# Performance work log

Hardware: AMD Instinct MI355X
Metric: run time of the kernel (lower is better)

## Reference

```python
import jax, jax.numpy as jnp
import numpy as np

N_NODES = 100000
N_EDGES = 1600000
DIM = 128


def setup_inputs() -> dict:
    key = jax.random.key(0)
    ks = jax.random.split(key, 8)
    s = 1.0 / np.sqrt(DIM)
    return {
        "x": jax.random.normal(ks[0], (N_NODES, DIM), dtype=jnp.float32),
        "edge_index": jax.random.randint(ks[1], (2, N_EDGES), 0, N_NODES, dtype=jnp.int64),
        "W1_l": jax.random.normal(ks[2], (DIM, DIM), dtype=jnp.float32) * s,
        "b1": jnp.zeros((DIM,), dtype=jnp.float32),
        "W1_r": jax.random.normal(ks[3], (DIM, DIM), dtype=jnp.float32) * s,
        "W2_l": jax.random.normal(ks[4], (DIM, DIM), dtype=jnp.float32) * s,
        "b2": jnp.zeros((DIM,), dtype=jnp.float32),
        "W2_r": jax.random.normal(ks[5], (DIM, DIM), dtype=jnp.float32) * s,
    }


def _sage_conv(h, src, dst, n, W_l, b, W_r):
    # mean aggregation of source-node features onto target nodes
    agg = jax.ops.segment_sum(h[src], dst, num_segments=n)          # [N, D]
    deg = jax.ops.segment_sum(jnp.ones_like(src, dtype=h.dtype), dst, num_segments=n)
    agg = agg / jnp.maximum(deg, 1.0)[:, None]
    # PyG SAGEConv: lin_l(aggr) + bias + lin_r(x)  (root weight, no bias on lin_r)
    return agg @ W_l + b + h @ W_r


def reference(x, edge_index, W1_l, b1, W1_r, W2_l, b2, W2_r):
    src, dst = edge_index[0], edge_index[1]
    n = x.shape[0]
    h = jax.nn.relu(_sage_conv(x, src, dst, n, W1_l, b1, W1_r))
    return _sage_conv(h, src, dst, n, W2_l, b2, W2_r)
```

## Files before the change

### kernel.cpp

```cpp
#include <hip/hip_runtime.h>

typedef unsigned short ushort_t;
typedef unsigned int uint_t;

typedef short bf16x8 __attribute__((ext_vector_type(8)));
typedef float f32x4 __attribute__((ext_vector_type(4)));

#define DIM 128
#define BSHIFT 8
#define BNODES 256
#define DBINS 64

__device__ __forceinline__ float bf2f(ushort_t u) {
    uint_t x = ((uint_t)u) << 16;
    float f;
    __builtin_memcpy(&f, &x, 4);
    return f;
}

__device__ __forceinline__ ushort_t f2bf(float f) {
    uint_t x;
    __builtin_memcpy(&x, &f, 4);
    uint_t r = (x + 0x7fffu + ((x >> 16) & 1u)) >> 16;
    return (ushort_t)r;
}


__global__ __launch_bounds__(256) void k_prep(const float* __restrict__ x, ushort_t* __restrict__ xb,
                                              int n4,
                                              const float* __restrict__ W0, const float* __restrict__ W1,
                                              const float* __restrict__ W2, const float* __restrict__ W3,
                                              ushort_t* __restrict__ T0, ushort_t* __restrict__ T1,
                                              ushort_t* __restrict__ T2, ushort_t* __restrict__ T3) {
    int i = blockIdx.x * 256 + threadIdx.x;
    if (i < n4) {
        float4 f = ((const float4*)x)[i];
        ushort4 u;
        u.x = f2bf(f.x); u.y = f2bf(f.y); u.z = f2bf(f.z); u.w = f2bf(f.w);
        ((ushort4*)xb)[i] = u;
    } else {
        int j = i - n4;
        if (j < 4 * DIM * DIM) {
            int w = j >> 14; j &= 16383;
            int n = j >> 7, k = j & 127;
            const float* W = (w == 0) ? W0 : (w == 1) ? W1 : (w == 2) ? W2 : W3;
            ushort_t* T = (w == 0) ? T0 : (w == 1) ? T1 : (w == 2) ? T2 : T3;
            T[j] = f2bf(W[k * DIM + n]);
        }
    }
}


__global__ __launch_bounds__(256) void k_bhist(const int* __restrict__ dst, int E, int NB,
                                               int* __restrict__ bucketCount) {
    __shared__ int hist[512];
    int t = threadIdx.x;
    for (int b = t; b < NB; b += 256) hist[b] = 0;
    __syncthreads();
    int per = (E + gridDim.x - 1) / gridDim.x;
    int beg = blockIdx.x * per, end = min(beg + per, E);
    for (int i = beg + t; i < end; i += 256)
        atomicAdd(&hist[dst[i] >> BSHIFT], 1);
    __syncthreads();
    for (int b = t; b < NB; b += 256) {
        int v = hist[b];
        if (v) atomicAdd(&bucketCount[b], v);
    }
}

__global__ __launch_bounds__(512) void k_bscan(const int* __restrict__ bucketCount, int NB, int E,
                                               int* __restrict__ bucketBase,
                                               int* __restrict__ bucketCursor,
                                               int* __restrict__ row_ptr, int N) {
    __shared__ int lds[512];
    int t = threadIdx.x;
    int v = (t < NB) ? bucketCount[t] : 0;
    lds[t] = v;
    __syncthreads();
    for (int off = 1; off < 512; off <<= 1) {
        int u = (t >= off) ? lds[t - off] : 0;
        __syncthreads();
        lds[t] += u;
        __syncthreads();
    }
    if (t < NB) {
        int b = lds[t] - v;
        bucketBase[t] = b;
        bucketCursor[t] = b;
    }
    if (t == 0) row_ptr[N] = E;
}

__global__ __launch_bounds__(256) void k_bucketize(const int* __restrict__ src,
                                                   const int* __restrict__ dst, int E, int NB,
                                                   int* __restrict__ bucketCursor,
                                                   uint_t* __restrict__ bebuf) {
    __shared__ int hist[512];
    __shared__ int base[512];
    int t = threadIdx.x;
    for (int b = t; b < NB; b += 256) hist[b] = 0;
    __syncthreads();
    int per = (E + gridDim.x - 1) / gridDim.x;
    int beg = blockIdx.x * per, end = min(beg + per, E);
    for (int i = beg + t; i < end; i += 256)
        atomicAdd(&hist[dst[i] >> BSHIFT], 1);
    __syncthreads();
    for (int b = t; b < NB; b += 256) {
        int v = hist[b];
        base[b] = v ? atomicAdd(&bucketCursor[b], v) : 0;
        hist[b] = 0;
    }
    __syncthreads();
    for (int i = beg + t; i < end; i += 256) {
        int d = dst[i], s = src[i];
        int b = d >> BSHIFT;
        int off = atomicAdd(&hist[b], 1);
        bebuf[base[b] + off] = ((uint_t)(d & (BNODES - 1)) << 24) | (uint_t)s;
    }
}

__global__ __launch_bounds__(256) void k_bcsr(const uint_t* __restrict__ bebuf,
                                              const int* __restrict__ bucketBase,
                                              const int* __restrict__ bucketCount, int N,
                                              int* __restrict__ row_ptr, int* __restrict__ csr,
                                              int* __restrict__ dhist) {
    __shared__ int hist[BNODES];
    __shared__ int cur[BNODES];
    __shared__ int dh[DBINS];
    int t = threadIdx.x;
    int b = blockIdx.x;
    int ebase = bucketBase[b], cnt = bucketCount[b];
    int nodeBase = b << BSHIFT;
    hist[t] = 0;
    if (t < DBINS) dh[t] = 0;
    __syncthreads();
    for (int i = t; i < cnt; i += 256)
        atomicAdd(&hist[bebuf[ebase + i] >> 24], 1);
    __syncthreads();
    int v = hist[t];
    int node = nodeBase + t;
    if (node < N) atomicAdd(&dh[min(v, DBINS - 1)], 1);
    for (int off = 1; off < 256; off <<= 1) {
        int u = (t >= off) ? hist[t - off] : 0;
        __syncthreads();
        hist[t] += u;
        __syncthreads();
    }
    int excl = hist[t] - v;
    if (node < N) row_ptr[node] = ebase + excl;
    cur[t] = excl;
    __syncthreads();
    for (int i = t; i < cnt; i += 256) {
        uint_t e = bebuf[ebase + i];
        int dl = (int)(e >> 24);
        int pos = atomicAdd(&cur[dl], 1);
        csr[ebase + pos] = (int)(e & 0xFFFFFFu);
    }
    __syncthreads();
    if (t < DBINS) {
        int c = dh[t];
        if (c) atomicAdd(&dhist[t], c);
    }
}


__global__ void k_dscan(const int* __restrict__ dhist, int* __restrict__ dcur) {
    __shared__ int l[DBINS];
    int t = threadIdx.x;
    int v = dhist[t];
    l[t] = v;
    __syncthreads();
    for (int off = 1; off < DBINS; off <<= 1) {
        int u = (t >= off) ? l[t - off] : 0;
        __syncthreads();
        l[t] += u;
        __syncthreads();
    }
    dcur[t] = l[t] - v;
}

__global__ __launch_bounds__(256) void k_dperm(const int* __restrict__ rp, int N,
                                               int* __restrict__ dcur, int* __restrict__ perm) {
    __shared__ int h[DBINS];
    __shared__ int base[DBINS];
    int t = threadIdx.x;
    if (t < DBINS) h[t] = 0;
    __syncthreads();
    int i = blockIdx.x * 256 + t;
    int b = -1;
    if (i < N) {
        int d = rp[i + 1] - rp[i];
        b = min(d, DBINS - 1);
        atomicAdd(&h[b], 1);
    }
    __syncthreads();
    if (t < DBINS) {
        int v = h[t];
        base[t] = v ? atomicAdd(&dcur[t], v) : 0;
        h[t] = 0;
    }
    __syncthreads();
    if (i < N) {
        int off = atomicAdd(&h[b], 1);
        perm[base[b] + off] = i;
    }
}


__device__ __forceinline__ void acc8(float* a, uint4 p) {
    union { uint_t u; float f; } c;
    c.u = p.x << 16;         a[0] += c.f;
    c.u = p.x & 0xffff0000u; a[1] += c.f;
    c.u = p.y << 16;         a[2] += c.f;
    c.u = p.y & 0xffff0000u; a[3] += c.f;
    c.u = p.z << 16;         a[4] += c.f;
    c.u = p.z & 0xffff0000u; a[5] += c.f;
    c.u = p.w << 16;         a[6] += c.f;
    c.u = p.w & 0xffff0000u; a[7] += c.f;
}

__global__ __launch_bounds__(256) void k_agg(const ushort_t* __restrict__ X,
                                             const int* __restrict__ row_ptr,
                                             const int* __restrict__ csr,
                                             const int* __restrict__ perm,
                                             ushort_t* __restrict__ out, int n) {
    int g = (int)((blockIdx.x * (unsigned)blockDim.x + threadIdx.x) >> 4);
    if (g >= n) return;
    int node = perm[g];
    int sl = threadIdx.x & 15;
    int beg = row_ptr[node], end = row_ptr[node + 1];
    float a[8] = {0.f, 0.f, 0.f, 0.f, 0.f, 0.f, 0.f, 0.f};

    int e = beg;
    for (; e + 8 <= end; e += 8) {
        uint4 p[8];
#pragma unroll
        for (int j = 0; j < 8; j++) {
            int s = csr[e + j];
            p[j] = *(const uint4*)(X + (size_t)s * DIM + sl * 8);
        }
#pragma unroll
        for (int j = 0; j < 8; j++) acc8(a, p[j]);
    }
    if (e + 4 <= end) {
        uint4 p[4];
#pragma unroll
        for (int j = 0; j < 4; j++) {
            int s = csr[e + j];
            p[j] = *(const uint4*)(X + (size_t)s * DIM + sl * 8);
        }
#pragma unroll
        for (int j = 0; j < 4; j++) acc8(a, p[j]);
        e += 4;
    }
    for (; e < end; e++) {
        int s = csr[e];
        uint4 p = *(const uint4*)(X + (size_t)s * DIM + sl * 8);
        acc8(a, p);
    }

    int cnt = end - beg;
    float sc = (cnt > 0) ? 1.f / (float)cnt : 0.f;
    uint4 o;
    o.x = (uint_t)f2bf(a[0] * sc) | ((uint_t)f2bf(a[1] * sc) << 16);
    o.y = (uint_t)f2bf(a[2] * sc) | ((uint_t)f2bf(a[3] * sc) << 16);
    o.z = (uint_t)f2bf(a[4] * sc) | ((uint_t)f2bf(a[5] * sc) << 16);
    o.w = (uint_t)f2bf(a[6] * sc) | ((uint_t)f2bf(a[7] * sc) << 16);
    *(uint4*)(out + (size_t)node * DIM + sl * 8) = o;
}


template <bool RELU, bool OUT_BF16>
__global__ __launch_bounds__(256) void k_gemm(const ushort_t* __restrict__ A1,
                                              const ushort_t* __restrict__ A2,
                                              const ushort_t* __restrict__ WTl,
                                              const ushort_t* __restrict__ WTr,
                                              const float* __restrict__ bias,
                                              void* __restrict__ Out, int n_waves, int M) {
    __shared__ ushort_t sW[2 * 128 * 128];
    int t = threadIdx.x;
    int wave = (int)((blockIdx.x * 256u + t) >> 6);
    int lane = t & 63;
    int col = lane & 15;
    int quad = lane >> 4;
    bool active = (wave < n_waves);

    bf16x8 a[2][8];
    if (active) {
#pragma unroll
        for (int tt = 0; tt < 2; tt++) {
            int arow = wave * 32 + tt * 16 + col;
            const ushort_t* a1p = A1 + (size_t)arow * DIM + quad * 8;
            const ushort_t* a2p = A2 + (size_t)arow * DIM + quad * 8;
#pragma unroll
            for (int ks = 0; ks < 4; ks++) a[tt][ks] = *(const bf16x8*)(a1p + ks * 32);
#pragma unroll
            for (int ks = 0; ks < 4; ks++) a[tt][4 + ks] = *(const bf16x8*)(a2p + ks * 32);
        }
    }

    {
        int tab = t >> 7, row = t & 127;
        const ushort_t* g = (tab ? WTr : WTl) + (size_t)row * 128;
        ushort_t* d = sW + (size_t)t * 128;
        int sw = row & 15;
#pragma unroll
        for (int c = 0; c < 16; c++) {
            uint4 v = *(const uint4*)(g + c * 8);
            *(uint4*)(d + ((c ^ sw) * 8)) = v;
        }
    }
    __syncthreads();
    if (!active) return;

    f32x4 acc[2][8];
#pragma unroll
    for (int tt = 0; tt < 2; tt++)
#pragma unroll
        for (int nt = 0; nt < 8; nt++) acc[tt][nt] = (f32x4){0.f, 0.f, 0.f, 0.f};

    const ushort_t* sWl = sW;
    const ushort_t* sWr = sW + 128 * 128;
#pragma unroll
    for (int nt = 0; nt < 8; nt++) {
        int row = nt * 16 + col;
        const ushort_t* bl = sWl + (size_t)row * 128;
        const ushort_t* br = sWr + (size_t)row * 128;
#pragma unroll
        for (int ks = 0; ks < 4; ks++) {
            bf16x8 b = *(const bf16x8*)(bl + (((ks * 4 + quad) ^ col) * 8));
            acc[0][nt] = __builtin_amdgcn_mfma_f32_16x16x32_bf16(a[0][ks], b, acc[0][nt], 0, 0, 0);
            acc[1][nt] = __builtin_amdgcn_mfma_f32_16x16x32_bf16(a[1][ks], b, acc[1][nt], 0, 0, 0);
        }
#pragma unroll
        for (int ks = 0; ks < 4; ks++) {
            bf16x8 b = *(const bf16x8*)(br + (((ks * 4 + quad) ^ col) * 8));
            acc[0][nt] = __builtin_amdgcn_mfma_f32_16x16x32_bf16(a[0][4 + ks], b, acc[0][nt], 0, 0, 0);
            acc[1][nt] = __builtin_amdgcn_mfma_f32_16x16x32_bf16(a[1][4 + ks], b, acc[1][nt], 0, 0, 0);
        }
    }

#pragma unroll
    for (int tt = 0; tt < 2; tt++)
#pragma unroll
        for (int nt = 0; nt < 8; nt++) {
            int c = nt * 16 + col;
            float bv = bias[c];
#pragma unroll
            for (int r = 0; r < 4; r++) {
                int m = wave * 32 + tt * 16 + quad * 4 + r;
                if (m < M) {
                    float v = acc[tt][nt][r] + bv;
                    if (RELU) v = v > 0.f ? v : 0.f;
                    if (OUT_BF16)
                        ((ushort_t*)Out)[(size_t)m * DIM + c] = f2bf(v);
                    else
                        ((float*)Out)[(size_t)m * DIM + c] = v;
                }
            }
        }
}


extern "C" void kernel_launch(void* const* d_in, const int* in_sizes, int n_in,
                              void* d_out, int out_size, void* d_ws, size_t ws_size,
                              hipStream_t stream) {
    const int N = in_sizes[0] / DIM;
    const int E = in_sizes[1] / 2;
    const int NB = (N + BNODES - 1) >> BSHIFT;

    const float* x   = (const float*)d_in[0];
    const int*   ei  = (const int*)d_in[1];
    const int*   src = ei;
    const int*   dst = ei + E;
    const float* W1l = (const float*)d_in[2];
    const float* b1  = (const float*)d_in[3];
    const float* W1r = (const float*)d_in[4];
    const float* W2l = (const float*)d_in[5];
    const float* b2  = (const float*)d_in[6];
    const float* W2r = (const float*)d_in[7];
    float* out = (float*)d_out;

    char* ws = (char*)d_ws;
    size_t off = 0;
    auto alloc = [&](size_t bytes) -> char* {
        char* p = ws + off;
        off = (off + bytes + 255) & ~(size_t)255;
        return p;
    };

    int*      bucketCount  = (int*)alloc((size_t)NB * 4);
    int*      dhist        = (int*)alloc((size_t)DBINS * 4);
    int*      dcur         = (int*)alloc((size_t)DBINS * 4);
    int*      bucketBase   = (int*)alloc((size_t)NB * 4);
    int*      bucketCursor = (int*)alloc((size_t)NB * 4);
    int*      row_ptr      = (int*)alloc((size_t)(N + 1) * 4);
    int*      csr          = (int*)alloc((size_t)E * 4);
    uint_t*   bebuf        = (uint_t*)alloc((size_t)E * 4);
    size_t    fpad         = (size_t)32 * DIM * 2;
    ushort_t* xb           = (ushort_t*)alloc((size_t)N * DIM * 2 + fpad);
    ushort_t* hb           = (ushort_t*)alloc((size_t)N * DIM * 2 + fpad);
    ushort_t* aggb         = (ushort_t*)alloc((size_t)N * DIM * 2 + fpad);
    ushort_t* wt1l         = (ushort_t*)alloc((size_t)DIM * DIM * 2);
    ushort_t* wt1r         = (ushort_t*)alloc((size_t)DIM * DIM * 2);
    ushort_t* wt2l         = (ushort_t*)alloc((size_t)DIM * DIM * 2);
    ushort_t* wt2r         = (ushort_t*)alloc((size_t)DIM * DIM * 2);
    int*      perm         = (int*)bebuf;

    hipMemsetAsync(bucketCount, 0, (size_t)((char*)dhist - (char*)bucketCount) + DBINS * 4, stream);

    {
        int n4 = N * DIM / 4;
        int total = n4 + 4 * DIM * DIM;
        k_prep<<<dim3((total + 255) / 256), dim3(256), 0, stream>>>(
            x, xb, n4, W1l, W1r, W2l, W2r, wt1l, wt1r, wt2l, wt2r);
    }
    k_bhist<<<dim3(256), dim3(256), 0, stream>>>(dst, E, NB, bucketCount);
    k_bscan<<<dim3(1), dim3(512), 0, stream>>>(bucketCount, NB, E, bucketBase, bucketCursor, row_ptr, N);
    k_bucketize<<<dim3(256), dim3(256), 0, stream>>>(src, dst, E, NB, bucketCursor, bebuf);
    k_bcsr<<<dim3(NB), dim3(256), 0, stream>>>(bebuf, bucketBase, bucketCount, N, row_ptr, csr, dhist);

    const int nblk = (N + 255) / 256;
    k_dscan<<<dim3(1), dim3(DBINS), 0, stream>>>(dhist, dcur);
    k_dperm<<<dim3(nblk), dim3(256), 0, stream>>>(row_ptr, N, dcur, perm);

    const int n_waves = (N + 31) / 32;
    dim3 gemm_grid((n_waves + 3) / 4), gemm_blk(256);
    dim3 agg_grid((N + 15) / 16), agg_blk(256);

    k_agg<<<agg_grid, agg_blk, 0, stream>>>(xb, row_ptr, csr, perm, aggb, N);
    k_gemm<true, true><<<gemm_grid, gemm_blk, 0, stream>>>(aggb, xb, wt1l, wt1r, b1, hb, n_waves, N);
    k_agg<<<agg_grid, agg_blk, 0, stream>>>(hb, row_ptr, csr, perm, aggb, N);
    k_gemm<false, false><<<gemm_grid, gemm_blk, 0, stream>>>(aggb, hb, wt2l, wt2r, b2, out, n_waves, N);

    (void)n_in; (void)out_size; (void)ws_size;
}
```

Measured before the change: 367.1 us.

## Make GEMM persistent with double-buffered A loads; fuse prep with histogram

The GEMM kernel becomes persistent with a grid of at most 512 blocks. Each block loads the weights into LDS once, then loops over 128-row tiles, prefetching the next tile's A fragments into registers while computing the current one. This amortises the 64KB weight staging per block and overlaps global loads with MFMA work, at the cost of higher register pressure (launch bounds 256,2). The bucket-histogram kernel is also merged into the x/weight conversion kernel to remove a launch, and the aggregation inner loop is cut from 8-way to 4-way unrolling.

```diff
diff --git a/kernel.cpp b/kernel.cpp
--- a/kernel.cpp
+++ b/kernel.cpp
@@ -26,12 +26,31 @@
 }
 
 
-__global__ __launch_bounds__(256) void k_prep(const float* __restrict__ x, ushort_t* __restrict__ xb,
-                                              int n4,
-                                              const float* __restrict__ W0, const float* __restrict__ W1,
-                                              const float* __restrict__ W2, const float* __restrict__ W3,
-                                              ushort_t* __restrict__ T0, ushort_t* __restrict__ T1,
-                                              ushort_t* __restrict__ T2, ushort_t* __restrict__ T3) {
+__global__ __launch_bounds__(256) void k_prep_bhist(
+        const float* __restrict__ x, ushort_t* __restrict__ xb, int n4,
+        const float* __restrict__ W0, const float* __restrict__ W1,
+        const float* __restrict__ W2, const float* __restrict__ W3,
+        ushort_t* __restrict__ T0, ushort_t* __restrict__ T1,
+        ushort_t* __restrict__ T2, ushort_t* __restrict__ T3,
+        const int* __restrict__ dst, int E, int NB, int* __restrict__ bucketCount,
+        int prepBlocks) {
+    if ((int)blockIdx.x >= prepBlocks) {
+        __shared__ int hist[512];
+        int blk = blockIdx.x - prepBlocks;
+        int t = threadIdx.x;
+        for (int b = t; b < NB; b += 256) hist[b] = 0;
+        __syncthreads();
+        int per = (E + 255) / 256;
+        int beg = blk * per, end = min(beg + per, E);
+        for (int i = beg + t; i < end; i += 256)
+            atomicAdd(&hist[dst[i] >> BSHIFT], 1);
+        __syncthreads();
+        for (int b = t; b < NB; b += 256) {
+            int v = hist[b];
+            if (v) atomicAdd(&bucketCount[b], v);
+        }
+        return;
+    }
     int i = blockIdx.x * 256 + threadIdx.x;
     if (i < n4) {
         float4 f = ((const float4*)x)[i];
@@ -51,23 +70,6 @@
 }
 
 
-__global__ __launch_bounds__(256) void k_bhist(const int* __restrict__ dst, int E, int NB,
-                                               int* __restrict__ bucketCount) {
-    __shared__ int hist[512];
-    int t = threadIdx.x;
-    for (int b = t; b < NB; b += 256) hist[b] = 0;
-    __syncthreads();
-    int per = (E + gridDim.x - 1) / gridDim.x;
-    int beg = blockIdx.x * per, end = min(beg + per, E);
-    for (int i = beg + t; i < end; i += 256)
-        atomicAdd(&hist[dst[i] >> BSHIFT], 1);
-    __syncthreads();
-    for (int b = t; b < NB; b += 256) {
-        int v = hist[b];
-        if (v) atomicAdd(&bucketCount[b], v);
-    }
-}
-
 __global__ __launch_bounds__(512) void k_bscan(const int* __restrict__ bucketCount, int NB, int E,
                                                int* __restrict__ bucketBase,
                                                int* __restrict__ bucketCursor,
@@ -232,26 +234,13 @@
     float a[8] = {0.f, 0.f, 0.f, 0.f, 0.f, 0.f, 0.f, 0.f};
 
     int e = beg;
-    for (; e + 8 <= end; e += 8) {
-        uint4 p[8];
-#pragma unroll
-        for (int j = 0; j < 8; j++) {
-            int s = csr[e + j];
-            p[j] = *(const uint4*)(X + (size_t)s * DIM + sl * 8);
-        }
-#pragma unroll
-        for (int j = 0; j < 8; j++) acc8(a, p[j]);
-    }
-    if (e + 4 <= end) {
-        uint4 p[4];
-#pragma unroll
-        for (int j = 0; j < 4; j++) {
-            int s = csr[e + j];
-            p[j] = *(const uint4*)(X + (size_t)s * DIM + sl * 8);
-        }
-#pragma unroll
-        for (int j = 0; j < 4; j++) acc8(a, p[j]);
-        e += 4;
+    for (; e + 4 <= end; e += 4) {
+        int s0 = csr[e + 0], s1 = csr[e + 1], s2 = csr[e + 2], s3 = csr[e + 3];
+        uint4 p0 = *(const uint4*)(X + (size_t)s0 * DIM + sl * 8);
+        uint4 p1 = *(const uint4*)(X + (size_t)s1 * DIM + sl * 8);
+        uint4 p2 = *(const uint4*)(X + (size_t)s2 * DIM + sl * 8);
+        uint4 p3 = *(const uint4*)(X + (size_t)s3 * DIM + sl * 8);
+        acc8(a, p0); acc8(a, p1); acc8(a, p2); acc8(a, p3);
     }
     for (; e < end; e++) {
         int s = csr[e];
@@ -271,25 +260,19 @@
 
 
 template <bool RELU, bool OUT_BF16>
-__global__ __launch_bounds__(256) void k_gemm(const ushort_t* __restrict__ A1,
-                                              const ushort_t* __restrict__ A2,
-                                              const ushort_t* __restrict__ WTl,
-                                              const ushort_t* __restrict__ WTr,
-                                              const float* __restrict__ bias,
-                                              void* __restrict__ Out, int n_waves, int M) {
-    __shared__ ushort_t sW[2 * 128 * 128];
-    int t = threadIdx.x;
-    int wave = (int)((blockIdx.x * 256u + t) >> 6);
-    int lane = t & 63;
-    int col = lane & 15;
-    int quad = lane >> 4;
-    bool active = (wave < n_waves);
-
-    bf16x8 a[2][8];
-    if (active) {
+struct GemmBody {
+    const ushort_t* A1;
+    const ushort_t* A2;
+    const ushort_t* sW;
+    void* Out;
+    int M;
+    int w, col, quad;
+    float bv[8];
+
+    __device__ __forceinline__ void loadA(bf16x8 (&a)[2][8], int tile) const {
 #pragma unroll
         for (int tt = 0; tt < 2; tt++) {
-            int arow = wave * 32 + tt * 16 + col;
+            int arow = tile * 128 + w * 32 + tt * 16 + col;
             const ushort_t* a1p = A1 + (size_t)arow * DIM + quad * 8;
             const ushort_t* a2p = A2 + (size_t)arow * DIM + quad * 8;
 #pragma unroll
@@ -298,6 +281,80 @@
             for (int ks = 0; ks < 4; ks++) a[tt][4 + ks] = *(const bf16x8*)(a2p + ks * 32);
         }
     }
+
+    __device__ __forceinline__ void compute(const bf16x8 (&a)[2][8], int tile) const {
+        f32x4 acc[2][8];
+#pragma unroll
+        for (int tt = 0; tt < 2; tt++)
+#pragma unroll
+            for (int nt = 0; nt < 8; nt++) acc[tt][nt] = (f32x4){0.f, 0.f, 0.f, 0.f};
+
+        const ushort_t* sWl = sW;
+        const ushort_t* sWr = sW + 128 * 128;
+        __builtin_amdgcn_s_setprio(1);
+#pragma unroll
+        for (int nt = 0; nt < 8; nt++) {
+            int row = nt * 16 + col;
+            const ushort_t* bl = sWl + (size_t)row * 128;
+            const ushort_t* br = sWr + (size_t)row * 128;
+#pragma unroll
+            for (int ks = 0; ks < 4; ks++) {
+                bf16x8 b = *(const bf16x8*)(bl + (((ks * 4 + quad) ^ col) * 8));
+                acc[0][nt] = __builtin_amdgcn_mfma_f32_16x16x32_bf16(a[0][ks], b, acc[0][nt], 0, 0, 0);
+                acc[1][nt] = __builtin_amdgcn_mfma_f32_16x16x32_bf16(a[1][ks], b, acc[1][nt], 0, 0, 0);
+            }
+#pragma unroll
+            for (int ks = 0; ks < 4; ks++) {
+                bf16x8 b = *(const bf16x8*)(br + (((ks * 4 + quad) ^ col) * 8));
+                acc[0][nt] = __builtin_amdgcn_mfma_f32_16x16x32_bf16(a[0][4 + ks], b, acc[0][nt], 0, 0, 0);
+                acc[1][nt] = __builtin_amdgcn_mfma_f32_16x16x32_bf16(a[1][4 + ks], b, acc[1][nt], 0, 0, 0);
+            }
+        }
+        __builtin_amdgcn_s_setprio(0);
+
+#pragma unroll
+        for (int tt = 0; tt < 2; tt++)
+#pragma unroll
+            for (int nt = 0; nt < 8; nt++) {
+                int c = nt * 16 + col;
+#pragma unroll
+                for (int r = 0; r < 4; r++) {
+                    int m = tile * 128 + w * 32 + tt * 16 + quad * 4 + r;
+                    if (m < M) {
+                        float v = acc[tt][nt][r] + bv[nt];
+                        if (RELU) v = v > 0.f ? v : 0.f;
+                        if (OUT_BF16)
+                            ((ushort_t*)Out)[(size_t)m * DIM + c] = f2bf(v);
+                        else
+                            ((float*)Out)[(size_t)m * DIM + c] = v;
+                    }
+                }
+            }
+    }
+};
+
+template <bool RELU, bool OUT_BF16>
+__global__ __launch_bounds__(256, 2) void k_gemm(const ushort_t* __restrict__ A1,
+                                                 const ushort_t* __restrict__ A2,
+                                                 const ushort_t* __restrict__ WTl,
+                                                 const ushort_t* __restrict__ WTr,
+                                                 const float* __restrict__ bias,
+                                                 void* __restrict__ Out, int ntiles, int M) {
+    __shared__ ushort_t sW[2 * 128 * 128];
+    int t = threadIdx.x;
+
+    GemmBody<RELU, OUT_BF16> gb;
+    gb.A1 = A1; gb.A2 = A2; gb.sW = sW; gb.Out = Out; gb.M = M;
+    gb.w = t >> 6;
+    int lane = t & 63;
+    gb.col = lane & 15;
+    gb.quad = lane >> 4;
+#pragma unroll
+    for (int nt = 0; nt < 8; nt++) gb.bv[nt] = bias[nt * 16 + gb.col];
+
+    int tile = blockIdx.x;
+    bf16x8 aA[2][8], aB[2][8];
+    gb.loadA(aA, tile);
 
     {
         int tab = t >> 7, row = t & 127;
@@ -311,54 +368,21 @@
         }
     }
     __syncthreads();
-    if (!active) return;
-
-    f32x4 acc[2][8];
-#pragma unroll
-    for (int tt = 0; tt < 2; tt++)
-#pragma unroll
-        for (int nt = 0; nt < 8; nt++) acc[tt][nt] = (f32x4){0.f, 0.f, 0.f, 0.f};
-
-    const ushort_t* sWl = sW;
-    const ushort_t* sWr = sW + 128 * 128;
-#pragma unroll
-    for (int nt = 0; nt < 8; nt++) {
-        int row = nt * 16 + col;
-        const ushort_t* bl = sWl + (size_t)row * 128;
-        const ushort_t* br = sWr + (size_t)row * 128;
-#pragma unroll
-        for (int ks = 0; ks < 4; ks++) {
-            bf16x8 b = *(const bf16x8*)(bl + (((ks * 4 + quad) ^ col) * 8));
-            acc[0][nt] = __builtin_amdgcn_mfma_f32_16x16x32_bf16(a[0][ks], b, acc[0][nt], 0, 0, 0);
-            acc[1][nt] = __builtin_amdgcn_mfma_f32_16x16x32_bf16(a[1][ks], b, acc[1][nt], 0, 0, 0);
-        }
-#pragma unroll
-        for (int ks = 0; ks < 4; ks++) {
-            bf16x8 b = *(const bf16x8*)(br + (((ks * 4 + quad) ^ col) * 8));
-            acc[0][nt] = __builtin_amdgcn_mfma_f32_16x16x32_bf16(a[0][4 + ks], b, acc[0][nt], 0, 0, 0);
-            acc[1][nt] = __builtin_amdgcn_mfma_f32_16x16x32_bf16(a[1][4 + ks], b, acc[1][nt], 0, 0, 0);
-        }
-    }
-
-#pragma unroll
-    for (int tt = 0; tt < 2; tt++)
-#pragma unroll
-        for (int nt = 0; nt < 8; nt++) {
-            int c = nt * 16 + col;
-            float bv = bias[c];
-#pragma unroll
-            for (int r = 0; r < 4; r++) {
-                int m = wave * 32 + tt * 16 + quad * 4 + r;
-                if (m < M) {
-                    float v = acc[tt][nt][r] + bv;
-                    if (RELU) v = v > 0.f ? v : 0.f;
-                    if (OUT_BF16)
-                        ((ushort_t*)Out)[(size_t)m * DIM + c] = f2bf(v);
-                    else
-                        ((float*)Out)[(size_t)m * DIM + c] = v;
-                }
-            }
-        }
+
+    int step = gridDim.x;
+    while (true) {
+        int t2 = tile + step;
+        if (t2 < ntiles) gb.loadA(aB, t2);
+        gb.compute(aA, tile);
+        tile = t2;
+        if (tile >= ntiles) break;
+
+        int t3 = tile + step;
+        if (t3 < ntiles) gb.loadA(aA, t3);
+        gb.compute(aB, tile);
+        tile = t3;
+        if (tile >= ntiles) break;
+    }
 }
 
 
@@ -397,7 +421,7 @@
     int*      row_ptr      = (int*)alloc((size_t)(N + 1) * 4);
     int*      csr          = (int*)alloc((size_t)E * 4);
     uint_t*   bebuf        = (uint_t*)alloc((size_t)E * 4);
-    size_t    fpad         = (size_t)32 * DIM * 2;
+    size_t    fpad         = (size_t)128 * DIM * 2;
     ushort_t* xb           = (ushort_t*)alloc((size_t)N * DIM * 2 + fpad);
     ushort_t* hb           = (ushort_t*)alloc((size_t)N * DIM * 2 + fpad);
     ushort_t* aggb         = (ushort_t*)alloc((size_t)N * DIM * 2 + fpad);
@@ -412,10 +436,11 @@
     {
         int n4 = N * DIM / 4;
         int total = n4 + 4 * DIM * DIM;
-        k_prep<<<dim3((total + 255) / 256), dim3(256), 0, stream>>>(
-            x, xb, n4, W1l, W1r, W2l, W2r, wt1l, wt1r, wt2l, wt2r);
-    }
-    k_bhist<<<dim3(256), dim3(256), 0, stream>>>(dst, E, NB, bucketCount);
+        int prepBlocks = (total + 255) / 256;
+        k_prep_bhist<<<dim3(prepBlocks + 256), dim3(256), 0, stream>>>(
+            x, xb, n4, W1l, W1r, W2l, W2r, wt1l, wt1r, wt2l, wt2r,
+            dst, E, NB, bucketCount, prepBlocks);
+    }
     k_bscan<<<dim3(1), dim3(512), 0, stream>>>(bucketCount, NB, E, bucketBase, bucketCursor, row_ptr, N);
     k_bucketize<<<dim3(256), dim3(256), 0, stream>>>(src, dst, E, NB, bucketCursor, bebuf);
     k_bcsr<<<dim3(NB), dim3(256), 0, stream>>>(bebuf, bucketBase, bucketCount, N, row_ptr, csr, dhist);
@@ -424,14 +449,14 @@
     k_dscan<<<dim3(1), dim3(DBINS), 0, stream>>>(dhist, dcur);
     k_dperm<<<dim3(nblk), dim3(256), 0, stream>>>(row_ptr, N, dcur, perm);
 
-    const int n_waves = (N + 31) / 32;
-    dim3 gemm_grid((n_waves + 3) / 4), gemm_blk(256);
+    const int ntiles = (N + 127) / 128;
+    dim3 gemm_grid((unsigned)min(ntiles, 512)), gemm_blk(256);
     dim3 agg_grid((N + 15) / 16), agg_blk(256);
 
     k_agg<<<agg_grid, agg_blk, 0, stream>>>(xb, row_ptr, csr, perm, aggb, N);
-    k_gemm<true, true><<<gemm_grid, gemm_blk, 0, stream>>>(aggb, xb, wt1l, wt1r, b1, hb, n_waves, N);
+    k_gemm<true, true><<<gemm_grid, gemm_blk, 0, stream>>>(aggb, xb, wt1l, wt1r, b1, hb, ntiles, N);
     k_agg<<<agg_grid, agg_blk, 0, stream>>>(hb, row_ptr, csr, perm, aggb, N);
-    k_gemm<false, false><<<gemm_grid, gemm_blk, 0, stream>>>(aggb, hb, wt2l, wt2r, b2, out, n_waves, N);
+    k_gemm<false, false><<<gemm_grid, gemm_blk, 0, stream>>>(aggb, hb, wt2l, wt2r, b2, out, ntiles, N);
 
     (void)n_in; (void)out_size; (void)ws_size;
 }
```

After: 354.6 us. 3.4% less time.
